# Kernel tuning notes

Hardware: AMD Instinct MI355X
Metric: run time of the kernel (lower is better)

The kernel has to match this reference:

```python
import jax, jax.numpy as jnp
import numpy as np

N_HEADS = 4
D_K = 64

def setup_inputs() -> dict:
    key = jax.random.key(0)
    k1, k2, k3 = jax.random.split(key, 3)
    B, C, H, W = 16, 256, 32, 32
    x = jax.random.normal(k1, (B, C, H, W), dtype=jnp.float32)
    # Linear(C, 3*n_heads*d_k) stored as [in, out] for x @ W
    w_proj = jax.random.normal(k2, (C, 3 * N_HEADS * D_K), dtype=jnp.float32) * (1.0 / np.sqrt(C))
    b_proj = jnp.zeros((3 * N_HEADS * D_K,), dtype=jnp.float32)
    w_out = jax.random.normal(k3, (N_HEADS * D_K, C), dtype=jnp.float32) * (1.0 / np.sqrt(N_HEADS * D_K))
    b_out = jnp.zeros((C,), dtype=jnp.float32)
    return {"x": x, "w_proj": w_proj, "b_proj": b_proj, "w_out": w_out, "b_out": b_out}

def reference(x, w_proj, b_proj, w_out, b_out):
    B, C, H, W = x.shape
    S = H * W
    scale = D_K ** -0.5
    xs = x.reshape(B, C, S).transpose(0, 2, 1)            # [B, S, C]
    qkv = (xs @ w_proj + b_proj).reshape(B, S, N_HEADS, 3 * D_K)
    q, k, v = jnp.split(qkv, 3, axis=3)                    # each [B, S, H, dk]
    attn = jnp.einsum('bihd,bjhd->bijh', q, k) * scale     # [B, S, S, heads]
    attn = jax.nn.softmax(attn, axis=2)
    o = jnp.einsum('bijh,bjhd->bihd', attn, v)             # [B, S, heads, dk]
    o = o.reshape(B, S, N_HEADS * D_K)
    res = o @ w_out + b_out + xs                           # [B, S, C]
    return res.transpose(0, 2, 1).reshape(B, C, H, W)
```

## Files before the change

### kernel.cpp

```cpp
#include <hip/hip_runtime.h>
#include <math.h>

#define B_  16
#define C_  256
#define S_  1024
#define NH  4
#define DK  64
#define P3  768
#define ND  256

typedef unsigned short u16;
typedef unsigned int   u32;
typedef float  f32x4  __attribute__((ext_vector_type(4)));
typedef short  bf16x8 __attribute__((ext_vector_type(8)));

#define MFMA16(a, b, c) __builtin_amdgcn_mfma_f32_16x16x32_bf16(a, b, c, 0, 0, 0)

#define QSCALE 0.1803368801111137f

#define WAITVM(N) asm volatile("s_waitcnt vmcnt(" #N ")" ::: "memory")
#define BARRIER() asm volatile("s_barrier" ::: "memory")

#if __has_builtin(__builtin_amdgcn_exp2f)
#define EXP2F(x) __builtin_amdgcn_exp2f(x)
#else
#define EXP2F(x) exp2f(x)
#endif

__device__ __forceinline__ u16 f2bf(float f) {
    union { float f; u32 u; } x; x.f = f;
    u32 r = x.u + 0x7fffu + ((x.u >> 16) & 1u);
    return (u16)(r >> 16);
}

__device__ __forceinline__ u32 cvtpk(float lo, float hi) {
    u32 r;
    asm("v_cvt_pk_bf16_f32 %0, %1, %2" : "=v"(r) : "v"(lo), "v"(hi));
    return r;
}

__device__ __forceinline__ void stage16(const u16* g, u16* l) {
    __builtin_amdgcn_global_load_lds(
        (const __attribute__((address_space(1))) void*)g,
        (__attribute__((address_space(3))) void*)l, 16, 0, 0);
}

__global__ __launch_bounds__(256) void transpose_w(
    const float* __restrict__ wp, u16* __restrict__ wpT,
    const float* __restrict__ wo, u16* __restrict__ woT)
{
    const int z = blockIdx.z;
    const int Cc = z ? 256 : 768;
    if ((int)blockIdx.x * 64 >= Cc) return;
    const float* src = z ? wo : wp;
    u16* dst = z ? woT : wpT;
    const int R = 256;

    __shared__ float T[64][65];
    const int tid = threadIdx.x;
    const int c0 = blockIdx.x * 64, r0 = blockIdx.y * 64;

    const int l64 = tid & 63, rr0 = tid >> 6;
    #pragma unroll
    for (int t = 0; t < 16; ++t) {
        int rr = rr0 + t * 4;
        T[rr][l64] = src[(size_t)(r0 + rr) * Cc + c0 + l64];
    }
    __syncthreads();
    const int rp = tid & 31;
    const int cb = tid >> 5;
    #pragma unroll
    for (int t = 0; t < 8; ++t) {
        int c = cb + t * 8;
        u32 lo = f2bf(T[2 * rp][c]);
        u32 hi = f2bf(T[2 * rp + 1][c]);
        *(u32*)&dst[(size_t)(c0 + c) * R + r0 + 2 * rp] = lo | (hi << 16);
    }
}

__global__ __launch_bounds__(256, 2) void qkv_fused(
    const float* __restrict__ x, const u16* __restrict__ wpT,
    const float* __restrict__ bp, u16* __restrict__ qo,
    u16* __restrict__ ko, u16* __restrict__ vo)
{
    __shared__ __align__(16) u16 SM[40960];

    const int tid = threadIdx.x;
    const int w = tid >> 6, lane = tid & 63;
    const int n_ = lane & 15, quad = lane >> 4;

    const int id  = blockIdx.x;
    const int nid = (id & 7) * 64 + (id >> 3);
    const int hd  = nid & 3;
    const int g   = nid >> 2;
    const int s0  = (g & 7) * 128;
    const int b   = g >> 3;
    const int bh  = b * NH + hd;

    const int kq8  = tid >> 5;
    const int row4 = tid & 31;
    const float* xb = x + ((size_t)b * C_ + kq8 * 8) * S_ + s0 + row4 * 4;

    int awaddr[4];
    {
        const int kc = kq8 >> 2, quadk = kq8 & 3;
        #pragma unroll
        for (int j = 0; j < 4; ++j) {
            int row = row4 * 4 + j;
            awaddr[j] = ((row >> 4) * 2 + kc) * 512 + quadk * 128 +
                        ((((row & 15) + (row >> 4)) & 15) * 8);
        }
    }

    const u16* brp[3];
    #pragma unroll
    for (int i = 0; i < 3; ++i)
        brp[i] = wpT + (size_t)(hd * 192 + (w * 3 + i) * 16 + n_) * C_ + quad * 8;

    f32x4 acc[2][12];
    #pragma unroll
    for (int am = 0; am < 2; ++am)
        #pragma unroll
        for (int nf = 0; nf < 12; ++nf)
            #pragma unroll
            for (int r = 0; r < 4; ++r) acc[am][nf][r] = 0.f;

    float4 av[8];

    #pragma unroll
    for (int ci = 0; ci < 8; ++ci)
        av[ci] = *(const float4*)(xb + (size_t)ci * S_);
    {
        u16* Bs0 = SM + 8192;
        #pragma unroll
        for (int i = 0; i < 3; ++i) {
            stage16(brp[i],      Bs0 + ((w * 3 + i) * 2 + 0) * 512);
            stage16(brp[i] + 32, Bs0 + ((w * 3 + i) * 2 + 1) * 512);
        }
    }
    #pragma unroll
    for (int j = 0; j < 4; ++j) {
        union { bf16x8 v; u32 u[4]; } pk;
        pk.u[0] = cvtpk(av[0][j], av[1][j]);
        pk.u[1] = cvtpk(av[2][j], av[3][j]);
        pk.u[2] = cvtpk(av[4][j], av[5][j]);
        pk.u[3] = cvtpk(av[6][j], av[7][j]);
        *(bf16x8*)&SM[awaddr[j]] = pk.v;
    }
    __syncthreads();

    #pragma unroll
    for (int p = 0; p < 4; ++p) {
        u16* As_ = SM + (p & 1) * 20480;
        u16* Bs_ = As_ + 8192;
        u16* An  = SM + ((p + 1) & 1) * 20480;
        u16* Bn  = An + 8192;

        if (p < 3) {
            #pragma unroll
            for (int ci = 0; ci < 8; ++ci)
                av[ci] = *(const float4*)(xb + ((size_t)(p + 1) * 64 + ci) * S_);
            #pragma unroll
            for (int i = 0; i < 3; ++i) {
                stage16(brp[i] + (p + 1) * 64,      Bn + ((w * 3 + i) * 2 + 0) * 512);
                stage16(brp[i] + (p + 1) * 64 + 32, Bn + ((w * 3 + i) * 2 + 1) * 512);
            }
        }

        #pragma unroll
        for (int kc = 0; kc < 2; ++kc) {
            bf16x8 af0 = *(const bf16x8*)&As_[((2 * w + 0) * 2 + kc) * 512 +
                                              quad * 128 + (((n_ + 2 * w + 0) & 15) * 8)];
            bf16x8 af1 = *(const bf16x8*)&As_[((2 * w + 1) * 2 + kc) * 512 +
                                              quad * 128 + (((n_ + 2 * w + 1) & 15) * 8)];
            #pragma unroll
            for (int nf = 0; nf < 12; ++nf) {
                bf16x8 bf = *(const bf16x8*)&Bs_[(nf * 2 + kc) * 512 + lane * 8];
                acc[0][nf] = MFMA16(af0, bf, acc[0][nf]);
                acc[1][nf] = MFMA16(af1, bf, acc[1][nf]);
            }
        }

        if (p < 3) {
            #pragma unroll
            for (int j = 0; j < 4; ++j) {
                union { bf16x8 v; u32 u[4]; } pk;
                pk.u[0] = cvtpk(av[0][j], av[1][j]);
                pk.u[1] = cvtpk(av[2][j], av[3][j]);
                pk.u[2] = cvtpk(av[4][j], av[5][j]);
                pk.u[3] = cvtpk(av[6][j], av[7][j]);
                *(bf16x8*)&An[awaddr[j]] = pk.v;
            }
        }
        __syncthreads();
    }

    float bias[12];
    #pragma unroll
    for (int nf = 0; nf < 12; ++nf) bias[nf] = bp[hd * 192 + nf * 16 + n_];

    u16* Cq = SM;
    u16* Ck = SM + 9216;
    u16* Cv = SM + 18432;

    #pragma unroll
    for (int am = 0; am < 2; ++am) {
        int row0 = w * 32 + am * 16 + quad * 4;
        #pragma unroll
        for (int nf = 0; nf < 4; ++nf)
            #pragma unroll
            for (int r = 0; r < 4; ++r)
                Cq[(row0 + r) * 72 + nf * 16 + n_] =
                    f2bf((acc[am][nf][r] + bias[nf]) * QSCALE);
        #pragma unroll
        for (int nf = 4; nf < 8; ++nf)
            #pragma unroll
            for (int r = 0; r < 4; ++r)
                Ck[(row0 + r) * 72 + (nf - 4) * 16 + n_] =
                    f2bf(acc[am][nf][r] + bias[nf]);
        int colb = w * 32 + am * 16 + quad * 4;
        #pragma unroll
        for (int nf = 8; nf < 12; ++nf)
            #pragma unroll
            for (int r = 0; r < 4; ++r)
                Cv[((nf - 8) * 16 + n_) * 136 + colb + r] =
                    f2bf(acc[am][nf][r] + bias[nf]);
    }
    __syncthreads();

    #pragma unroll
    for (int t = 0; t < 4; ++t) {
        int ii = tid + t * 256;
        int row = ii >> 3, c8 = (ii & 7) * 8;
        *(bf16x8*)&qo[((size_t)bh * S_ + s0 + row) * DK + c8] =
            *(const bf16x8*)&Cq[row * 72 + c8];
        {
            int jt = (s0 + row) >> 6;
            int r  = row & 63;
            int nb = ((r >> 5) & 1) + 2 * ((r >> 2) & 1);
            int nk = ((r >> 3) & 3) * 4 + (r & 3);
            int h  = c8 >> 5, qd = (c8 >> 3) & 3;
            int lk = nk + 16 * qd;
            *(bf16x8*)&ko[((size_t)(bh * 16 + jt) * 8 + nb * 2 + h) * 512 + lk * 8] =
                *(const bf16x8*)&Ck[row * 72 + c8];
        }
        {
            int vrow = ii >> 4, vc8 = (ii & 15) * 8;
            int sg = s0 + vc8;
            int jt = sg >> 6;
            int cs = sg & 63;
            int h  = cs >> 5, qd = (cs >> 3) & 3;
            int nd = vrow >> 4, nv = vrow & 15;
            int lv = nv + 16 * qd;
            *(bf16x8*)&vo[((size_t)(bh * 16 + jt) * 8 + nd * 2 + h) * 512 + lv * 8] =
                *(const bf16x8*)&Cv[vrow * 136 + vc8];
        }
    }
}

__global__ __launch_bounds__(256, 2) void attn_mfma(
    const u16* __restrict__ q, const u16* __restrict__ k,
    const u16* __restrict__ vt, u16* __restrict__ obf)
{
    __shared__ __align__(16) u16 SM[9216];

    const int tid = threadIdx.x;
    const int w = tid >> 6, lane = tid & 63;
    const int n_ = lane & 15, quad = lane >> 4;

    const int id  = blockIdx.x;
    const int nid = (id & 7) * 64 + (id >> 3);
    const int i0  = (nid & 7) * 128;
    const int bh  = nid >> 3;
    const int hd  = bh & 3;
    const int b   = bh >> 2;

    bf16x8 qf[2][2];
    #pragma unroll
    for (int am = 0; am < 2; ++am) {
        const u16* qrow = q + ((size_t)bh * S_ + i0 + w * 32 + am * 16 + n_) * DK;
        qf[am][0] = *(const bf16x8*)&qrow[quad * 8];
        qf[am][1] = *(const bf16x8*)&qrow[32 + quad * 8];
    }

    union { bf16x8 v; u32 u[4]; } ones_;
    #pragma unroll
    for (int i = 0; i < 4; ++i) ones_.u[i] = 0x3F803F80u;
    const bf16x8 onesf = ones_.v;

    const u16* kfb = k  + (size_t)bh * 16 * 4096 + lane * 8;
    const u16* vfb = vt + (size_t)bh * 16 * 4096 + lane * 8;

    f32x4 oacc[2][4];
    f32x4 acc_sum[2];
    #pragma unroll
    for (int am = 0; am < 2; ++am) {
        #pragma unroll
        for (int nd = 0; nd < 4; ++nd)
            #pragma unroll
            for (int r = 0; r < 4; ++r) oacc[am][nd][r] = 0.f;
        #pragma unroll
        for (int r = 0; r < 4; ++r) acc_sum[am][r] = 0.f;
    }

    bf16x8 kf[2][8], vf[2][8];
    bf16x8 pa[2][2];

    #pragma unroll
    for (int f = 0; f < 8; ++f)
        kf[0][f] = *(const bf16x8*)(kfb + f * 512);

    #pragma unroll 16
    for (int t = 0; t < 16; ++t) {
        const int cur = t & 1, nxt = (t + 1) & 1;
        if (t < 15) {
            #pragma unroll
            for (int f = 0; f < 8; ++f)
                kf[nxt][f] = *(const bf16x8*)(kfb + (size_t)(t + 1) * 4096 + f * 512);
        }
        #pragma unroll
        for (int f = 0; f < 8; ++f)
            vf[cur][f] = *(const bf16x8*)(vfb + (size_t)t * 4096 + f * 512);

        f32x4 sb[2][4];
        __builtin_amdgcn_s_setprio(1);
        #pragma unroll
        for (int nb = 0; nb < 4; ++nb) {
            #pragma unroll
            for (int am = 0; am < 2; ++am) {
                f32x4 a; a[0] = a[1] = a[2] = a[3] = 0.f;
                a = MFMA16(kf[cur][nb * 2 + 0], qf[am][0], a);
                a = MFMA16(kf[cur][nb * 2 + 1], qf[am][1], a);
                sb[am][nb] = a;
            }
        }

        if (t > 0) {
            const int prv = (t - 1) & 1;
            #pragma unroll
            for (int nd = 0; nd < 4; ++nd)
                #pragma unroll
                for (int am = 0; am < 2; ++am) {
                    oacc[am][nd] = MFMA16(vf[prv][nd * 2 + 0], pa[am][0], oacc[am][nd]);
                    oacc[am][nd] = MFMA16(vf[prv][nd * 2 + 1], pa[am][1], oacc[am][nd]);
                }
            #pragma unroll
            for (int am = 0; am < 2; ++am) {
                acc_sum[am] = MFMA16(onesf, pa[am][0], acc_sum[am]);
                acc_sum[am] = MFMA16(onesf, pa[am][1], acc_sum[am]);
            }
        }
        __builtin_amdgcn_s_setprio(0);

        #pragma unroll
        for (int am = 0; am < 2; ++am) {
            float pr[4][4];
            #pragma unroll
            for (int nb = 0; nb < 4; ++nb)
                #pragma unroll
                for (int r = 0; r < 4; ++r)
                    pr[nb][r] = EXP2F(sb[am][nb][r]);
            union { bf16x8 v; u32 u[4]; } p0, p1;
            p0.u[0] = cvtpk(pr[0][0], pr[0][1]);
            p0.u[1] = cvtpk(pr[0][2], pr[0][3]);
            p0.u[2] = cvtpk(pr[2][0], pr[2][1]);
            p0.u[3] = cvtpk(pr[2][2], pr[2][3]);
            p1.u[0] = cvtpk(pr[1][0], pr[1][1]);
            p1.u[1] = cvtpk(pr[1][2], pr[1][3]);
            p1.u[2] = cvtpk(pr[3][0], pr[3][1]);
            p1.u[3] = cvtpk(pr[3][2], pr[3][3]);
            pa[am][0] = p0.v;
            pa[am][1] = p1.v;
        }
    }

    {
        __builtin_amdgcn_s_setprio(1);
        #pragma unroll
        for (int nd = 0; nd < 4; ++nd)
            #pragma unroll
            for (int am = 0; am < 2; ++am) {
                oacc[am][nd] = MFMA16(vf[1][nd * 2 + 0], pa[am][0], oacc[am][nd]);
                oacc[am][nd] = MFMA16(vf[1][nd * 2 + 1], pa[am][1], oacc[am][nd]);
            }
        #pragma unroll
        for (int am = 0; am < 2; ++am) {
            acc_sum[am] = MFMA16(onesf, pa[am][0], acc_sum[am]);
            acc_sum[am] = MFMA16(onesf, pa[am][1], acc_sum[am]);
        }
        __builtin_amdgcn_s_setprio(0);
    }

    const float inv0 = 1.f / acc_sum[0][0];
    const float inv1 = 1.f / acc_sum[1][0];
    float inv[2] = {inv0, inv1};

    u16* eb = SM + w * 2304;
    #pragma unroll
    for (int am = 0; am < 2; ++am)
        #pragma unroll
        for (int nd = 0; nd < 4; ++nd) {
            uint2 uv;
            uv.x = cvtpk(oacc[am][nd][0] * inv[am], oacc[am][nd][1] * inv[am]);
            uv.y = cvtpk(oacc[am][nd][2] * inv[am], oacc[am][nd][3] * inv[am]);
            *(uint2*)&eb[(am * 16 + n_) * 72 + nd * 16 + quad * 4] = uv;
        }
    __syncthreads();
    #pragma unroll
    for (int t = 0; t < 4; ++t) {
        int ii = lane + t * 64;
        int row = ii >> 3, c8 = (ii & 7) * 8;
        *(bf16x8*)&obf[((size_t)b * S_ + i0 + w * 32 + row) * ND + hd * DK + c8] =
            *(const bf16x8*)&eb[row * 72 + c8];
    }
}

__global__ __launch_bounds__(256) void out_proj_mfma(
    const u16* __restrict__ obf, const u16* __restrict__ woT,
    const float* __restrict__ bo, const float* __restrict__ x,
    float* __restrict__ out)
{
    __shared__ __align__(16) u16 SM[24576];

    const int tid = threadIdx.x;
    const int w = tid >> 6, lane = tid & 63;
    const int n_ = lane & 15, quad = lane >> 4;

    const int id  = blockIdx.x;
    const int nid = (id & 7) * 64 + (id >> 3);
    const int c0  = (nid & 3) * 64;
    const int g   = nid >> 2;
    const int s0  = (g & 7) * 128;
    const int b   = g >> 3;

    const u16* ar  = woT + (size_t)(c0 + w * 16 + n_) * ND + quad * 8;
    const u16* br0 = obf + ((size_t)b * S_ + s0 + (2 * w + 0) * 16 + n_) * ND + quad * 8;
    const u16* br1 = obf + ((size_t)b * S_ + s0 + (2 * w + 1) * 16 + n_) * ND + quad * 8;

    f32x4 acc[2][4];
    #pragma unroll
    for (int nf = 0; nf < 2; ++nf)
        #pragma unroll
        for (int mb = 0; mb < 4; ++mb)
            #pragma unroll
            for (int r = 0; r < 4; ++r) acc[nf][mb][r] = 0.f;

    {
        u16* Bs_ = SM;
        u16* As_ = SM + 8192;
        stage16(br0,      Bs_ + (4 * w + 0) * 512);
        stage16(br0 + 32, Bs_ + (4 * w + 1) * 512);
        stage16(br1,      Bs_ + (4 * w + 2) * 512);
        stage16(br1 + 32, Bs_ + (4 * w + 3) * 512);
        stage16(ar,       As_ + (2 * w + 0) * 512);
        stage16(ar + 32,  As_ + (2 * w + 1) * 512);
    }

    #pragma unroll
    for (int p = 0; p < 4; ++p) {
        u16* Bs_ = SM + (p & 1) * 12288;
        u16* As_ = Bs_ + 8192;
        if (p < 3) {
            const int pk = (p + 1) * 64;
            u16* Bn = SM + ((p + 1) & 1) * 12288;
            u16* An = Bn + 8192;
            stage16(br0 + pk,      Bn + (4 * w + 0) * 512);
            stage16(br0 + pk + 32, Bn + (4 * w + 1) * 512);
            stage16(br1 + pk,      Bn + (4 * w + 2) * 512);
            stage16(br1 + pk + 32, Bn + (4 * w + 3) * 512);
            stage16(ar  + pk,      An + (2 * w + 0) * 512);
            stage16(ar  + pk + 32, An + (2 * w + 1) * 512);
            WAITVM(6);
        } else {
            WAITVM(0);
        }
        BARRIER();
        #pragma unroll
        for (int kc = 0; kc < 2; ++kc) {
            bf16x8 bf0 = *(const bf16x8*)&Bs_[((2 * w + 0) * 2 + kc) * 512 + lane * 8];
            bf16x8 bf1 = *(const bf16x8*)&Bs_[((2 * w + 1) * 2 + kc) * 512 + lane * 8];
            #pragma unroll
            for (int mb = 0; mb < 4; ++mb) {
                bf16x8 af = *(const bf16x8*)&As_[(mb * 2 + kc) * 512 + lane * 8];
                acc[0][mb] = MFMA16(af, bf0, acc[0][mb]);
                acc[1][mb] = MFMA16(af, bf1, acc[1][mb]);
            }
        }
        if (p < 3) BARRIER();
    }

    #pragma unroll
    for (int mb = 0; mb < 4; ++mb)
        #pragma unroll
        for (int r = 0; r < 4; ++r) {
            int c = c0 + mb * 16 + quad * 4 + r;
            float bias = bo[c];
            #pragma unroll
            for (int nf = 0; nf < 2; ++nf) {
                size_t idx = ((size_t)b * C_ + c) * S_ + s0 + w * 32 + nf * 16 + n_;
                out[idx] = acc[nf][mb][r] + bias + x[idx];
            }
        }
}

extern "C" void kernel_launch(void* const* d_in, const int* in_sizes, int n_in,
                              void* d_out, int out_size, void* d_ws, size_t ws_size,
                              hipStream_t stream) {
    const float* x  = (const float*)d_in[0];
    const float* wp = (const float*)d_in[1];
    const float* bp = (const float*)d_in[2];
    const float* wo = (const float*)d_in[3];
    const float* bo = (const float*)d_in[4];
    float* out = (float*)d_out;

    const size_t QKV_E = (size_t)B_ * NH * S_ * DK;
    u16* q   = (u16*)d_ws;
    u16* kk  = q   + QKV_E;
    u16* vtp = kk  + QKV_E;
    u16* obf = vtp + QKV_E;
    u16* wpT = obf + (size_t)B_ * S_ * ND;
    u16* woT = wpT + (size_t)P3 * C_;

    transpose_w  <<<dim3(12, 4, 2),  256, 0, stream>>>(wp, wpT, wo, woT);
    qkv_fused    <<<dim3(512, 1, 1), 256, 0, stream>>>(x, wpT, bp, q, kk, vtp);
    attn_mfma    <<<dim3(512, 1, 1), 256, 0, stream>>>(q, kk, vtp, obf);
    out_proj_mfma<<<dim3(512, 1, 1), 256, 0, stream>>>(obf, woT, bo, x, out);
}
```

Measured before the change: 123.7 us.

## Stage K/V tiles through LDS with a 4-slot async ring shared by warps

Each of the four warps used to load every K and V fragment straight from global memory into registers, so each warp fetched the whole tile. Now each warp stages a quarter of every K/V tile into LDS with stage16, using a 4-slot ring buffer two tiles ahead with vmcnt waits and barriers, and all warps read fragments from LDS. This cuts redundant global/L2 traffic fourfold and frees registers. In exchange it adds a barrier per iteration and grows LDS to 64KB per block, which may limit occupancy under launch_bounds(256,2).

Measured after the change: 122.9 us. No clear change (-0.7%).

```diff
diff --git a/kernel.cpp b/kernel.cpp
--- a/kernel.cpp
+++ b/kernel.cpp
@@ -262,7 +262,7 @@
     const u16* __restrict__ q, const u16* __restrict__ k,
     const u16* __restrict__ vt, u16* __restrict__ obf)
 {
-    __shared__ __align__(16) u16 SM[9216];
+    __shared__ __align__(16) u16 SM[32768];
 
     const int tid = threadIdx.x;
     const int w = tid >> 6, lane = tid & 63;
@@ -288,8 +288,8 @@
     for (int i = 0; i < 4; ++i) ones_.u[i] = 0x3F803F80u;
     const bf16x8 onesf = ones_.v;
 
-    const u16* kfb = k  + (size_t)bh * 16 * 4096 + lane * 8;
-    const u16* vfb = vt + (size_t)bh * 16 * 4096 + lane * 8;
+    const u16* ksrc = k  + (size_t)bh * 16 * 4096 + (2 * w) * 512 + lane * 8;
+    const u16* vsrc = vt + (size_t)bh * 16 * 4096 + (2 * w) * 512 + lane * 8;
 
     f32x4 oacc[2][4];
     f32x4 acc_sum[2];
@@ -303,47 +303,56 @@
         for (int r = 0; r < 4; ++r) acc_sum[am][r] = 0.f;
     }
 
-    bf16x8 kf[2][8], vf[2][8];
+    #pragma unroll
+    for (int tt = 0; tt < 2; ++tt) {
+        u16* Ks = SM + tt * 8192;
+        stage16(ksrc + (size_t)tt * 4096,       Ks + (2 * w + 0) * 512);
+        stage16(ksrc + (size_t)tt * 4096 + 512, Ks + (2 * w + 1) * 512);
+        stage16(vsrc + (size_t)tt * 4096,       Ks + 4096 + (2 * w + 0) * 512);
+        stage16(vsrc + (size_t)tt * 4096 + 512, Ks + 4096 + (2 * w + 1) * 512);
+    }
+
     bf16x8 pa[2][2];
 
-    #pragma unroll
-    for (int f = 0; f < 8; ++f)
-        kf[0][f] = *(const bf16x8*)(kfb + f * 512);
-
-    #pragma unroll 16
     for (int t = 0; t < 16; ++t) {
-        const int cur = t & 1, nxt = (t + 1) & 1;
-        if (t < 15) {
-            #pragma unroll
-            for (int f = 0; f < 8; ++f)
-                kf[nxt][f] = *(const bf16x8*)(kfb + (size_t)(t + 1) * 4096 + f * 512);
-        }
-        #pragma unroll
-        for (int f = 0; f < 8; ++f)
-            vf[cur][f] = *(const bf16x8*)(vfb + (size_t)t * 4096 + f * 512);
+        u16* Ks = SM + (t & 3) * 8192;
+        u16* Vp = SM + ((t + 3) & 3) * 8192 + 4096;
+        if (t < 15) WAITVM(4); else WAITVM(0);
+        BARRIER();
+        if (t < 14) {
+            u16* Kn = SM + ((t + 2) & 3) * 8192;
+            stage16(ksrc + (size_t)(t + 2) * 4096,       Kn + (2 * w + 0) * 512);
+            stage16(ksrc + (size_t)(t + 2) * 4096 + 512, Kn + (2 * w + 1) * 512);
+            stage16(vsrc + (size_t)(t + 2) * 4096,       Kn + 4096 + (2 * w + 0) * 512);
+            stage16(vsrc + (size_t)(t + 2) * 4096 + 512, Kn + 4096 + (2 * w + 1) * 512);
+        }
 
         f32x4 sb[2][4];
         __builtin_amdgcn_s_setprio(1);
         #pragma unroll
         for (int nb = 0; nb < 4; ++nb) {
+            bf16x8 kf0 = *(const bf16x8*)&Ks[(nb * 2 + 0) * 512 + lane * 8];
+            bf16x8 kf1 = *(const bf16x8*)&Ks[(nb * 2 + 1) * 512 + lane * 8];
             #pragma unroll
             for (int am = 0; am < 2; ++am) {
                 f32x4 a; a[0] = a[1] = a[2] = a[3] = 0.f;
-                a = MFMA16(kf[cur][nb * 2 + 0], qf[am][0], a);
-                a = MFMA16(kf[cur][nb * 2 + 1], qf[am][1], a);
+                a = MFMA16(kf0, qf[am][0], a);
+                a = MFMA16(kf1, qf[am][1], a);
                 sb[am][nb] = a;
             }
         }
 
         if (t > 0) {
-            const int prv = (t - 1) & 1;
-            #pragma unroll
-            for (int nd = 0; nd < 4; ++nd)
+            #pragma unroll
+            for (int nd = 0; nd < 4; ++nd) {
+                bf16x8 vf0 = *(const bf16x8*)&Vp[(nd * 2 + 0) * 512 + lane * 8];
+                bf16x8 vf1 = *(const bf16x8*)&Vp[(nd * 2 + 1) * 512 + lane * 8];
                 #pragma unroll
                 for (int am = 0; am < 2; ++am) {
-                    oacc[am][nd] = MFMA16(vf[prv][nd * 2 + 0], pa[am][0], oacc[am][nd]);
-                    oacc[am][nd] = MFMA16(vf[prv][nd * 2 + 1], pa[am][1], oacc[am][nd]);
+                    oacc[am][nd] = MFMA16(vf0, pa[am][0], oacc[am][nd]);
+                    oacc[am][nd] = MFMA16(vf1, pa[am][1], oacc[am][nd]);
                 }
+            }
             #pragma unroll
             for (int am = 0; am < 2; ++am) {
                 acc_sum[am] = MFMA16(onesf, pa[am][0], acc_sum[am]);
@@ -375,14 +384,18 @@
     }
 
     {
+        u16* Vp = SM + 3 * 8192 + 4096;
         __builtin_amdgcn_s_setprio(1);
         #pragma unroll
-        for (int nd = 0; nd < 4; ++nd)
+        for (int nd = 0; nd < 4; ++nd) {
+            bf16x8 vf0 = *(const bf16x8*)&Vp[(nd * 2 + 0) * 512 + lane * 8];
+            bf16x8 vf1 = *(const bf16x8*)&Vp[(nd * 2 + 1) * 512 + lane * 8];
             #pragma unroll
             for (int am = 0; am < 2; ++am) {
-                oacc[am][nd] = MFMA16(vf[1][nd * 2 + 0], pa[am][0], oacc[am][nd]);
-                oacc[am][nd] = MFMA16(vf[1][nd * 2 + 1], pa[am][1], oacc[am][nd]);
-            }
+                oacc[am][nd] = MFMA16(vf0, pa[am][0], oacc[am][nd]);
+                oacc[am][nd] = MFMA16(vf1, pa[am][1], oacc[am][nd]);
+            }
+        }
         #pragma unroll
         for (int am = 0; am < 2; ++am) {
             acc_sum[am] = MFMA16(onesf, pa[am][0], acc_sum[am]);
@@ -395,6 +408,7 @@
     const float inv1 = 1.f / acc_sum[1][0];
     float inv[2] = {inv0, inv1};
 
+    __syncthreads();
     u16* eb = SM + w * 2304;
     #pragma unroll
     for (int am = 0; am < 2; ++am)
```
